# Kernel optimization log

Hardware: AMD Instinct MI355X
Metric: run time of the kernel (lower is better)

The kernel has to match this reference:

```python
import jax, jax.numpy as jnp
import numpy as np


def _scale_relpos_1d(emb, new_side_length):
    # Linear interpolation WITHOUT corner alignment (half-pixel centers),
    # matching torch F.interpolate(mode='linear', align_corners=False).
    new_num = 2 * new_side_length - 1
    if new_num == emb.shape[0]:
        return emb
    return jax.image.resize(emb.astype(jnp.float32), (new_num, emb.shape[1]), method='linear').astype(emb.dtype)


def setup_inputs() -> dict:
    key = jax.random.key(0)
    k1, k2, k3 = jax.random.split(key, 3)
    B, H, W, C = 16, 64, 64, 80
    N = H * W
    return {
        'query_tokens': jax.random.normal(k1, (B, N, C), dtype=jnp.float32),
        'relpos_h_1d': jax.random.normal(k2, (2 * H - 1, C), dtype=jnp.float32) * 0.02,
        'relpos_w_1d': jax.random.normal(k3, (2 * W - 1, C), dtype=jnp.float32) * 0.02,
        'h': H,
        'w': W,
    }


def reference(query_tokens, relpos_h_1d, relpos_w_1d, h, w):
    b, n, c = query_tokens.shape
    # rescale learned tables if grid differs from base (no-op when sizes match)
    rpos_h = _scale_relpos_1d(relpos_h_1d, h)
    rpos_w = _scale_relpos_1d(relpos_w_1d, w)
    # relative index deltas: (h,h) and (w,w), values in [0, 2h-2] / [0, 2w-2]
    ih = jnp.arange(h)
    iw = jnp.arange(w)
    dh = ih[:, None] - ih[None, :] + (h - 1)
    dw = iw[:, None] - iw[None, :] + (w - 1)
    rpos_hhc = rpos_h[dh]  # (h, h, c)
    rpos_wwc = rpos_w[dw]  # (w, w, c)
    q = query_tokens.reshape(b, h, w, c)
    rh = jnp.einsum('bhwc,hjc->bhwj', q, rpos_hhc).reshape(b, n, h)  # per-row h-bias
    rw = jnp.einsum('bhwc,wic->bhwi', q, rpos_wwc).reshape(b, n, w)  # per-row w-bias
    # broadcast-add: (b,n,h,1) + (b,n,1,w) -> (b,n,h,w) -> (b,n,n)
    return (rh[:, :, :, None] + rw[:, :, None, :]).reshape(b, n, n)
```

## Files before the change

kernel.cpp:

```cpp
#include <hip/hip_runtime.h>

#define HH 64
#define WW 64
#define CC 80
#define NN (HH * WW)
#define G  16
#define RPW 79
#define SP  84

typedef float vf4 __attribute__((ext_vector_type(4)));

__global__ __launch_bounds__(256, 5) void relpos_fused_v6(
    const float* __restrict__ q,
    const float* __restrict__ ph,
    const float* __restrict__ pw,
    float* __restrict__ out)
{
    __shared__ float sh_q [G * CC];
    __shared__ float sh_pw[RPW * SP];

    const int blk = blockIdx.x;
    const int s   = blk & 3;
    const int hh  = (blk >> 2) & 63;
    const int b   = blk >> 8;
    const int ww0 = s * G;
    const int t   = threadIdx.x;

    const vf4* qin4 = reinterpret_cast<const vf4*>(
        q + ((size_t)b * NN + hh * 64 + ww0) * CC);
    vf4* shq4 = reinterpret_cast<vf4*>(sh_q);
    #pragma unroll
    for (int p = t; p < G * CC / 4; p += 256) shq4[p] = qin4[p];

    const vf4* pwsrc = reinterpret_cast<const vf4*>(pw + (size_t)ww0 * CC);
    vf4* shpw4 = reinterpret_cast<vf4*>(sh_pw);
    for (int p = t; p < RPW * (CC / 4); p += 256) {
        const int r  = p / 20;
        const int w4 = p % 20;
        shpw4[r * (SP / 4) + w4] = pwsrc[p];
    }
    __syncthreads();

    const int j = t & 63;
    const int w = t >> 6;
    const float* phrow = ph + (size_t)(hh + 63 - j) * CC;

    float acch[4] = {0.f, 0.f, 0.f, 0.f};
    float accw[4] = {0.f, 0.f, 0.f, 0.f};
    for (int c = 0; c < CC; c += 4) {
        vf4 hv = *reinterpret_cast<const vf4*>(phrow + c);
        #pragma unroll
        for (int k = 0; k < 4; ++k) {
            const int g = w + 4 * k;
            vf4 qv = *reinterpret_cast<const vf4*>(&sh_q[g * CC + c]);
            vf4 wv = *reinterpret_cast<const vf4*>(
                &sh_pw[(g + 63 - j) * SP + c]);
            acch[k] += qv.x * hv.x + qv.y * hv.y + qv.z * hv.z + qv.w * hv.w;
            accw[k] += qv.x * wv.x + qv.y * wv.y + qv.z * wv.z + qv.w * wv.w;
        }
    }

    vf4* out4 = reinterpret_cast<vf4*>(
        out + ((size_t)b * NN + hh * 64 + ww0) * NN);
    const int rwlane = 4 * (j & 15);
    const int rhbase = j >> 4;
    #pragma unroll
    for (int k = 0; k < 4; ++k) {
        const int g = w + 4 * k;
        const float w0 = __shfl(accw[k], rwlane + 0);
        const float w1 = __shfl(accw[k], rwlane + 1);
        const float w2 = __shfl(accw[k], rwlane + 2);
        const float w3 = __shfl(accw[k], rwlane + 3);
        float rh[16];
        #pragma unroll
        for (int it = 0; it < 16; ++it)
            rh[it] = __shfl(acch[k], it * 4 + rhbase);
        #pragma unroll
        for (int it = 0; it < 16; ++it) {
            vf4 o;
            o.x = rh[it] + w0; o.y = rh[it] + w1;
            o.z = rh[it] + w2; o.w = rh[it] + w3;
            __builtin_nontemporal_store(o, &out4[g * 1024 + it * 64 + j]);
        }
    }
}

extern "C" void kernel_launch(void* const* d_in, const int* in_sizes, int n_in,
                              void* d_out, int out_size, void* d_ws, size_t ws_size,
                              hipStream_t stream) {
    const float* q  = (const float*)d_in[0];
    const float* ph = (const float*)d_in[1];
    const float* pw = (const float*)d_in[2];
    float* out = (float*)d_out;

    const int B = in_sizes[0] / (NN * CC);
    dim3 grid(B * HH * (WW / G));
    relpos_fused_v6<<<grid, 256, 0, stream>>>(q, ph, pw, out);
}
```

Before: 196.6 us.

## Process full w-row per block and cache ph row in registers

Each block now computes all 64 w positions of one h row instead of 16, loading the whole pw table and the q row into shared memory once. The ph row for each thread is held in 20 vector registers and reused across 16 loop iterations, and the output is interleaved with compute per g. This cuts redundant global and shared loads of ph and pw. In exchange it uses more LDS and registers, lowering occupancy with fewer, larger blocks in an output-write-bound kernel.

```diff
diff --git a/kernel.cpp b/kernel.cpp
--- a/kernel.cpp
+++ b/kernel.cpp
@@ -4,83 +4,84 @@
 #define WW 64
 #define CC 80
 #define NN (HH * WW)
-#define G  16
-#define RPW 79
+#define NPW 127
 #define SP  84
 
 typedef float vf4 __attribute__((ext_vector_type(4)));
 
-__global__ __launch_bounds__(256, 5) void relpos_fused_v6(
+__global__ __launch_bounds__(256, 2) void relpos_fused_v7(
     const float* __restrict__ q,
     const float* __restrict__ ph,
     const float* __restrict__ pw,
     float* __restrict__ out)
 {
-    __shared__ float sh_q [G * CC];
-    __shared__ float sh_pw[RPW * SP];
+    __shared__ float sh_q [64 * CC];
+    __shared__ float sh_pw[NPW * SP];
 
     const int blk = blockIdx.x;
-    const int s   = blk & 3;
-    const int hh  = (blk >> 2) & 63;
-    const int b   = blk >> 8;
-    const int ww0 = s * G;
+    const int hh  = blk & 63;
+    const int b   = blk >> 6;
     const int t   = threadIdx.x;
+    const int j   = t & 63;
+    const int w   = t >> 6;
 
     const vf4* qin4 = reinterpret_cast<const vf4*>(
-        q + ((size_t)b * NN + hh * 64 + ww0) * CC);
+        q + ((size_t)b * NN + hh * 64) * CC);
     vf4* shq4 = reinterpret_cast<vf4*>(sh_q);
     #pragma unroll
-    for (int p = t; p < G * CC / 4; p += 256) shq4[p] = qin4[p];
+    for (int p = t; p < 64 * CC / 4; p += 256) shq4[p] = qin4[p];
 
-    const vf4* pwsrc = reinterpret_cast<const vf4*>(pw + (size_t)ww0 * CC);
+    const vf4* pwsrc = reinterpret_cast<const vf4*>(pw);
     vf4* shpw4 = reinterpret_cast<vf4*>(sh_pw);
-    for (int p = t; p < RPW * (CC / 4); p += 256) {
+    for (int p = t; p < NPW * (CC / 4); p += 256) {
         const int r  = p / 20;
-        const int w4 = p % 20;
-        shpw4[r * (SP / 4) + w4] = pwsrc[p];
+        const int c4 = p % 20;
+        shpw4[r * (SP / 4) + c4] = pwsrc[p];
     }
     __syncthreads();
 
-    const int j = t & 63;
-    const int w = t >> 6;
-    const float* phrow = ph + (size_t)(hh + 63 - j) * CC;
+    vf4 hv[20];
+    const vf4* phrow = reinterpret_cast<const vf4*>(
+        ph + (size_t)(hh + 63 - j) * CC);
+    #pragma unroll
+    for (int c = 0; c < 20; ++c) hv[c] = phrow[c];
 
-    float acch[4] = {0.f, 0.f, 0.f, 0.f};
-    float accw[4] = {0.f, 0.f, 0.f, 0.f};
-    for (int c = 0; c < CC; c += 4) {
-        vf4 hv = *reinterpret_cast<const vf4*>(phrow + c);
-        #pragma unroll
-        for (int k = 0; k < 4; ++k) {
-            const int g = w + 4 * k;
-            vf4 qv = *reinterpret_cast<const vf4*>(&sh_q[g * CC + c]);
-            vf4 wv = *reinterpret_cast<const vf4*>(
-                &sh_pw[(g + 63 - j) * SP + c]);
-            acch[k] += qv.x * hv.x + qv.y * hv.y + qv.z * hv.z + qv.w * hv.w;
-            accw[k] += qv.x * wv.x + qv.y * wv.y + qv.z * wv.z + qv.w * wv.w;
-        }
-    }
-
-    vf4* out4 = reinterpret_cast<vf4*>(
-        out + ((size_t)b * NN + hh * 64 + ww0) * NN);
+    vf4* outbase = reinterpret_cast<vf4*>(
+        out + ((size_t)b * NN + hh * 64) * NN);
     const int rwlane = 4 * (j & 15);
     const int rhbase = j >> 4;
-    #pragma unroll
-    for (int k = 0; k < 4; ++k) {
-        const int g = w + 4 * k;
-        const float w0 = __shfl(accw[k], rwlane + 0);
-        const float w1 = __shfl(accw[k], rwlane + 1);
-        const float w2 = __shfl(accw[k], rwlane + 2);
-        const float w3 = __shfl(accw[k], rwlane + 3);
+
+    for (int k = 0; k < 16; ++k) {
+        const int g = 4 * k + w;
+        const float* qrow = &sh_q[g * CC];
+        const float* wrow = &sh_pw[(size_t)(g + 63 - j) * SP];
+
+        float acch = 0.f, accw = 0.f;
+        #pragma unroll
+        for (int c = 0; c < 20; ++c) {
+            vf4 qv = *reinterpret_cast<const vf4*>(qrow + 4 * c);
+            vf4 wv = *reinterpret_cast<const vf4*>(wrow + 4 * c);
+            acch += qv.x * hv[c].x + qv.y * hv[c].y
+                  + qv.z * hv[c].z + qv.w * hv[c].w;
+            accw += qv.x * wv.x + qv.y * wv.y + qv.z * wv.z + qv.w * wv.w;
+        }
+
+        const float w0 = __shfl(accw, rwlane + 0);
+        const float w1 = __shfl(accw, rwlane + 1);
+        const float w2 = __shfl(accw, rwlane + 2);
+        const float w3 = __shfl(accw, rwlane + 3);
         float rh[16];
         #pragma unroll
         for (int it = 0; it < 16; ++it)
-            rh[it] = __shfl(acch[k], it * 4 + rhbase);
+            rh[it] = __shfl(acch, it * 4 + rhbase);
+
+        vf4* o4 = outbase + (size_t)g * 1024;
         #pragma unroll
         for (int it = 0; it < 16; ++it) {
             vf4 o;
             o.x = rh[it] + w0; o.y = rh[it] + w1;
             o.z = rh[it] + w2; o.w = rh[it] + w3;
-            __builtin_nontemporal_store(o, &out4[g * 1024 + it * 64 + j]);
+            __builtin_nontemporal_store(o, &o4[it * 64 + j]);
         }
     }
 }
@@ -94,6 +95,6 @@
     float* out = (float*)d_out;
 
     const int B = in_sizes[0] / (NN * CC);
-    dim3 grid(B * HH * (WW / G));
-    relpos_fused_v6<<<grid, 256, 0, stream>>>(q, ph, pw, out);
+    dim3 grid(B * HH);
+    relpos_fused_v7<<<grid, 256, 0, stream>>>(q, ph, pw, out);
 }
```

New measurement: 206.5 us. +5.0%, slower.

## Split fused kernel into dot-product pass and broadcast-write pass via workspace

Applied to the files above, without the earlier changes.

Splits the fused kernel into two launches. The first computes the per-row h and w bias dot products and writes them to a workspace buffer. The second reads those biases back and streams the large broadcast-add output with nontemporal stores. The goal is to decouple the compute-heavy phase from the store-bound phase so each can use its own occupancy. The cost is an extra launch plus a write and read of an intermediate buffer of about 33 MB. The fused kernel is kept as a fallback when the workspace is too small.

```diff
diff --git a/kernel.cpp b/kernel.cpp
--- a/kernel.cpp
+++ b/kernel.cpp
@@ -10,11 +10,11 @@
 
 typedef float vf4 __attribute__((ext_vector_type(4)));
 
-__global__ __launch_bounds__(256, 5) void relpos_fused_v6(
+__global__ __launch_bounds__(256, 5) void relpos_dots_k1(
     const float* __restrict__ q,
     const float* __restrict__ ph,
     const float* __restrict__ pw,
-    float* __restrict__ out)
+    float* __restrict__ ws)
 {
     __shared__ float sh_q [G * CC];
     __shared__ float sh_pw[RPW * SP];
@@ -36,8 +36,90 @@
     vf4* shpw4 = reinterpret_cast<vf4*>(sh_pw);
     for (int p = t; p < RPW * (CC / 4); p += 256) {
         const int r  = p / 20;
-        const int w4 = p % 20;
-        shpw4[r * (SP / 4) + w4] = pwsrc[p];
+        const int c4 = p % 20;
+        shpw4[r * (SP / 4) + c4] = pwsrc[p];
+    }
+    __syncthreads();
+
+    const int j = t & 63;
+    const int w = t >> 6;
+    const float* phrow = ph + (size_t)(hh + 63 - j) * CC;
+
+    float acch[4] = {0.f, 0.f, 0.f, 0.f};
+    float accw[4] = {0.f, 0.f, 0.f, 0.f};
+    for (int c = 0; c < CC; c += 4) {
+        vf4 hv = *reinterpret_cast<const vf4*>(phrow + c);
+        #pragma unroll
+        for (int k = 0; k < 4; ++k) {
+            const int g = w + 4 * k;
+            vf4 qv = *reinterpret_cast<const vf4*>(&sh_q[g * CC + c]);
+            vf4 wv = *reinterpret_cast<const vf4*>(
+                &sh_pw[(g + 63 - j) * SP + c]);
+            acch[k] += qv.x * hv.x + qv.y * hv.y + qv.z * hv.z + qv.w * hv.w;
+            accw[k] += qv.x * wv.x + qv.y * wv.y + qv.z * wv.z + qv.w * wv.w;
+        }
+    }
+    #pragma unroll
+    for (int k = 0; k < 4; ++k) {
+        const int g  = w + 4 * k;
+        const size_t bn = (size_t)b * NN + hh * 64 + ww0 + g;
+        ws[bn * 128 + j]      = acch[k];
+        ws[bn * 128 + 64 + j] = accw[k];
+    }
+}
+
+__global__ __launch_bounds__(256) void relpos_write_k2(
+    const float* __restrict__ ws,
+    float* __restrict__ out)
+{
+    const int t  = threadIdx.x;
+    const int j  = t & 63;
+    const int w  = t >> 6;
+    const size_t bn = (size_t)blockIdx.x * 4 + w;
+
+    const float* base = ws + bn * 128;
+    const vf4 rwv = *reinterpret_cast<const vf4*>(base + 64 + 4 * (j & 15));
+    const int rhb = j >> 4;
+    float rh[16];
+    #pragma unroll
+    for (int it = 0; it < 16; ++it) rh[it] = base[it * 4 + rhb];
+
+    vf4* o4 = reinterpret_cast<vf4*>(out) + bn * 1024;
+    #pragma unroll
+    for (int it = 0; it < 16; ++it) {
+        vf4 o;
+        o.x = rh[it] + rwv.x; o.y = rh[it] + rwv.y;
+        o.z = rh[it] + rwv.z; o.w = rh[it] + rwv.w;
+        __builtin_nontemporal_store(o, &o4[it * 64 + j]);
+    }
+}
+
+__global__ __launch_bounds__(256, 5) void relpos_fused_v6(
+    const float* __restrict__ q, const float* __restrict__ ph,
+    const float* __restrict__ pw, float* __restrict__ out)
+{
+    __shared__ float sh_q [G * CC];
+    __shared__ float sh_pw[RPW * SP];
+
+    const int blk = blockIdx.x;
+    const int s   = blk & 3;
+    const int hh  = (blk >> 2) & 63;
+    const int b   = blk >> 8;
+    const int ww0 = s * G;
+    const int t   = threadIdx.x;
+
+    const vf4* qin4 = reinterpret_cast<const vf4*>(
+        q + ((size_t)b * NN + hh * 64 + ww0) * CC);
+    vf4* shq4 = reinterpret_cast<vf4*>(sh_q);
+    #pragma unroll
+    for (int p = t; p < G * CC / 4; p += 256) shq4[p] = qin4[p];
+
+    const vf4* pwsrc = reinterpret_cast<const vf4*>(pw + (size_t)ww0 * CC);
+    vf4* shpw4 = reinterpret_cast<vf4*>(sh_pw);
+    for (int p = t; p < RPW * (CC / 4); p += 256) {
+        const int r  = p / 20;
+        const int c4 = p % 20;
+        shpw4[r * (SP / 4) + c4] = pwsrc[p];
     }
     __syncthreads();
 
@@ -94,6 +176,13 @@
     float* out = (float*)d_out;
 
     const int B = in_sizes[0] / (NN * CC);
-    dim3 grid(B * HH * (WW / G));
-    relpos_fused_v6<<<grid, 256, 0, stream>>>(q, ph, pw, out);
+    const size_t need = (size_t)B * NN * 128 * sizeof(float);
+
+    if (ws_size >= need) {
+        float* wsf = (float*)d_ws;
+        relpos_dots_k1<<<dim3(B * HH * (WW / G)), 256, 0, stream>>>(q, ph, pw, wsf);
+        relpos_write_k2<<<dim3(B * NN / 4), 256, 0, stream>>>(wsf, out);
+    } else {
+        relpos_fused_v6<<<dim3(B * HH * (WW / G)), 256, 0, stream>>>(q, ph, pw, out);
+    }
 }
```

Result: slower. 256.6 us (+30.6%).
